# Kernel optimization log

Measured on AMD Instinct MI355X. Metric: run time of the kernel, lower is better.

## Reference

```python
import jax, jax.numpy as jnp
import numpy as np

B, F, ND, NE = 1024, 1024, 256, 256

def setup_inputs() -> dict:
    key = jax.random.key(0)
    k1, k2, k3 = jax.random.split(key, 3)
    x = jax.random.normal(k1, (B, F), dtype=jnp.float32)
    # xavier-uniform-like init scale for (F+1, units)
    lim_d = float(np.sqrt(6.0 / (F + 1 + ND)))
    lim_e = float(np.sqrt(6.0 / (F + 1 + NE)))
    dilations = jax.random.uniform(k2, (F + 1, ND), minval=-lim_d, maxval=lim_d, dtype=jnp.float32)
    erosions = jax.random.uniform(k3, (F + 1, NE), minval=-lim_e, maxval=lim_e, dtype=jnp.float32)
    return {"x": x, "dilations": dilations, "erosions": erosions}

def reference(x, dilations, erosions):
    b = x.shape[0]
    # append a zero 'bias' feature -> (b, F+1)
    xb = jnp.concatenate([x, jnp.zeros((b, 1), dtype=x.dtype)], axis=1)
    # tropical matmuls: max-plus (dilation), min-minus (erosion)
    dilated = jnp.max(xb[:, :, None] + dilations[None, :, :], axis=1)   # (b, ND)
    eroded = jnp.min(xb[:, :, None] - erosions[None, :, :], axis=1)     # (b, NE)
    return jnp.concatenate([eroded, dilated], axis=1)
```

## Files before the change

kernel.cpp:

```cpp
#include <hip/hip_runtime.h>
#include <math.h>

#define BB   1024
#define FF   1024
#define NOUT 512
#define NW   256
#define BT   128
#define NT   64
#define KT   32

__global__ __launch_bounds__(256, 2) void trop_main(
    const float* __restrict__ x,
    const float* __restrict__ dil,
    const float* __restrict__ ero,
    float* __restrict__ dst,
    int ks, int ch, int direct)
{
    const int bx = blockIdx.x;
    const int by = blockIdx.y;
    const int bz = blockIdx.z;
    const bool is_ero = (bx < (NW / NT));
    const float* __restrict__ w = is_ero ? ero : dil;
    const int c0w = is_ero ? bx * NT : bx * NT - NW;
    const int r0 = by * BT;
    const float sgn = is_ero ? -1.0f : 1.0f;

    __shared__ float lds_x[KT][BT];
    __shared__ float lds_w[KT][NT];

    const int tid = threadIdx.x;
    const int cg = tid & 7;
    const int rg = tid >> 3;

    float acc[4][8];
#pragma unroll
    for (int i = 0; i < 4; ++i)
#pragma unroll
        for (int j = 0; j < 8; ++j) acc[i][j] = -INFINITY;

    const int fstart = bz * ch;
    const int nchunk = ch / KT;

    for (int kc = 0; kc < nchunk; ++kc) {
        const int fb = fstart + kc * KT;

#pragma unroll
        for (int it = 0; it < 4; ++it) {
            const int tt = tid + it * 256;
            const int r = tt & 127;
            const int g = tt >> 7;
            const float4 v = *(const float4*)(x + (size_t)(r0 + r) * FF + fb + g * 4);
            lds_x[g * 4 + 0][r] = sgn * v.x;
            lds_x[g * 4 + 1][r] = sgn * v.y;
            lds_x[g * 4 + 2][r] = sgn * v.z;
            lds_x[g * 4 + 3][r] = sgn * v.w;
        }
#pragma unroll
        for (int it = 0; it < 2; ++it) {
            const int tt = tid + it * 256;
            const int f = tt >> 4;
            const int c4 = tt & 15;
            *(float4*)&lds_w[f][c4 * 4] =
                *(const float4*)(w + (size_t)(fb + f) * NW + c0w + c4 * 4);
        }
        __syncthreads();

#pragma unroll
        for (int ff = 0; ff < KT; ff += 2) {
            const float4 x0 = *(const float4*)&lds_x[ff][rg << 2];
            const float4 x1 = *(const float4*)&lds_x[ff + 1][rg << 2];
            const float4 wa0 = *(const float4*)&lds_w[ff][cg << 3];
            const float4 wb0 = *(const float4*)&lds_w[ff][(cg << 3) + 4];
            const float4 wa1 = *(const float4*)&lds_w[ff + 1][cg << 3];
            const float4 wb1 = *(const float4*)&lds_w[ff + 1][(cg << 3) + 4];
            const float xr0[4] = {x0.x, x0.y, x0.z, x0.w};
            const float xr1[4] = {x1.x, x1.y, x1.z, x1.w};
            const float wc0[8] = {wa0.x, wa0.y, wa0.z, wa0.w, wb0.x, wb0.y, wb0.z, wb0.w};
            const float wc1[8] = {wa1.x, wa1.y, wa1.z, wa1.w, wb1.x, wb1.y, wb1.z, wb1.w};
#pragma unroll
            for (int i = 0; i < 4; ++i)
#pragma unroll
                for (int j = 0; j < 8; ++j) {
                    acc[i][j] = fmaxf(acc[i][j],
                                      fmaxf(xr0[i] + wc0[j], xr1[i] + wc1[j]));
                }
        }
        __syncthreads();
    }

    if (bz == ks - 1) {
        const float4 ba = *(const float4*)(w + (size_t)FF * NW + c0w + (cg << 3));
        const float4 bb = *(const float4*)(w + (size_t)FF * NW + c0w + (cg << 3) + 4);
        const float bc[8] = {ba.x, ba.y, ba.z, ba.w, bb.x, bb.y, bb.z, bb.w};
#pragma unroll
        for (int i = 0; i < 4; ++i)
#pragma unroll
            for (int j = 0; j < 8; ++j) acc[i][j] = fmaxf(acc[i][j], bc[j]);
    }

    float* base = direct ? dst : dst + (size_t)bz * (BB * NOUT);
    const int cglob = bx * NT + (cg << 3);
#pragma unroll
    for (int i = 0; i < 4; ++i) {
        const int row = r0 + (rg << 2) + i;
        float4 v0, v1;
        v0.x = sgn * acc[i][0]; v0.y = sgn * acc[i][1];
        v0.z = sgn * acc[i][2]; v0.w = sgn * acc[i][3];
        v1.x = sgn * acc[i][4]; v1.y = sgn * acc[i][5];
        v1.z = sgn * acc[i][6]; v1.w = sgn * acc[i][7];
        *(float4*)(base + (size_t)row * NOUT + cglob) = v0;
        *(float4*)(base + (size_t)row * NOUT + cglob + 4) = v1;
    }
}

__global__ __launch_bounds__(256) void trop_combine(
    const float* __restrict__ ws, float* __restrict__ out, int ks)
{
    const int i4 = blockIdx.x * blockDim.x + threadIdx.x;
    const int col4 = (i4 << 2) & (NOUT - 1);
    const bool ero = col4 < NW;
    const int stride4 = BB * NOUT / 4;
    float4 v = ((const float4*)ws)[i4];
    for (int z = 1; z < ks; ++z) {
        const float4 u = ((const float4*)ws)[(size_t)z * stride4 + i4];
        if (ero) {
            v.x = fminf(v.x, u.x); v.y = fminf(v.y, u.y);
            v.z = fminf(v.z, u.z); v.w = fminf(v.w, u.w);
        } else {
            v.x = fmaxf(v.x, u.x); v.y = fmaxf(v.y, u.y);
            v.z = fmaxf(v.z, u.z); v.w = fmaxf(v.w, u.w);
        }
    }
    ((float4*)out)[i4] = v;
}

extern "C" void kernel_launch(void* const* d_in, const int* in_sizes, int n_in,
                              void* d_out, int out_size, void* d_ws, size_t ws_size,
                              hipStream_t stream) {
    const float* x = (const float*)d_in[0];
    const float* dil = (const float*)d_in[1];
    const float* ero = (const float*)d_in[2];
    float* out = (float*)d_out;

    const size_t outbytes = (size_t)BB * NOUT * sizeof(float);
    int ks = 1;
    if (ws_size >= 8 * outbytes) ks = 8;
    else if (ws_size >= 4 * outbytes) ks = 4;
    else if (ws_size >= 2 * outbytes) ks = 2;

    if (ks > 1) {
        dim3 grid(NOUT / NT, BB / BT, ks);
        trop_main<<<grid, 256, 0, stream>>>(x, dil, ero, (float*)d_ws, ks, FF / ks, 0);
        const int n4 = BB * NOUT / 4;
        trop_combine<<<n4 / 256, 256, 0, stream>>>((const float*)d_ws, out, ks);
    } else {
        dim3 grid(NOUT / NT, BB / BT, 1);
        trop_main<<<grid, 256, 0, stream>>>(x, dil, ero, out, 1, FF, 1);
    }
}
```

Measured before the change: 90.91 us.

## Replace split-K workspace and combine pass with atomic min/max into output

```diff
diff --git a/kernel.cpp b/kernel.cpp
--- a/kernel.cpp
+++ b/kernel.cpp
@@ -8,22 +8,38 @@
 #define BT   128
 #define NT   64
 #define KT   32
+#define KS   16
+#define CH   (FF / KS)
+#define NCHUNK (CH / KT)
 
-__global__ __launch_bounds__(256, 2) void trop_main(
+__device__ __forceinline__ void atomMaxF(float* p, float v) {
+    if (v >= 0.0f) atomicMax((int*)p, __float_as_int(v));
+    else           atomicMin((unsigned int*)p, __float_as_uint(v));
+}
+__device__ __forceinline__ void atomMinF(float* p, float v) {
+    if (v >= 0.0f) atomicMin((int*)p, __float_as_int(v));
+    else           atomicMax((unsigned int*)p, __float_as_uint(v));
+}
+
+__global__ __launch_bounds__(256) void trop_init(float* __restrict__ out) {
+    const int i4 = blockIdx.x * 256 + threadIdx.x;
+    const int col = (i4 << 2) & (NOUT - 1);
+    const float v = (col < NW) ? INFINITY : -INFINITY;
+    float4 o; o.x = v; o.y = v; o.z = v; o.w = v;
+    ((float4*)out)[i4] = o;
+}
+
+template <bool IS_ERO>
+__global__ __launch_bounds__(256, 4) void trop_main(
     const float* __restrict__ x,
-    const float* __restrict__ dil,
-    const float* __restrict__ ero,
-    float* __restrict__ dst,
-    int ks, int ch, int direct)
+    const float* __restrict__ w,
+    float* __restrict__ out)
 {
     const int bx = blockIdx.x;
     const int by = blockIdx.y;
     const int bz = blockIdx.z;
-    const bool is_ero = (bx < (NW / NT));
-    const float* __restrict__ w = is_ero ? ero : dil;
-    const int c0w = is_ero ? bx * NT : bx * NT - NW;
+    const int c0w = bx * NT;
     const int r0 = by * BT;
-    const float sgn = is_ero ? -1.0f : 1.0f;
 
     __shared__ float lds_x[KT][BT];
     __shared__ float lds_w[KT][NT];
@@ -38,10 +54,10 @@
 #pragma unroll
         for (int j = 0; j < 8; ++j) acc[i][j] = -INFINITY;
 
-    const int fstart = bz * ch;
-    const int nchunk = ch / KT;
+    const int fstart = bz * CH;
 
-    for (int kc = 0; kc < nchunk; ++kc) {
+#pragma unroll
+    for (int kc = 0; kc < NCHUNK; ++kc) {
         const int fb = fstart + kc * KT;
 
 #pragma unroll
@@ -50,10 +66,10 @@
             const int r = tt & 127;
             const int g = tt >> 7;
             const float4 v = *(const float4*)(x + (size_t)(r0 + r) * FF + fb + g * 4);
-            lds_x[g * 4 + 0][r] = sgn * v.x;
-            lds_x[g * 4 + 1][r] = sgn * v.y;
-            lds_x[g * 4 + 2][r] = sgn * v.z;
-            lds_x[g * 4 + 3][r] = sgn * v.w;
+            lds_x[g * 4 + 0][r] = v.x;
+            lds_x[g * 4 + 1][r] = v.y;
+            lds_x[g * 4 + 2][r] = v.z;
+            lds_x[g * 4 + 3][r] = v.w;
         }
 #pragma unroll
         for (int it = 0; it < 2; ++it) {
@@ -81,14 +97,18 @@
             for (int i = 0; i < 4; ++i)
 #pragma unroll
                 for (int j = 0; j < 8; ++j) {
-                    acc[i][j] = fmaxf(acc[i][j],
-                                      fmaxf(xr0[i] + wc0[j], xr1[i] + wc1[j]));
+                    if (IS_ERO)
+                        acc[i][j] = fmaxf(acc[i][j],
+                                          fmaxf(wc0[j] - xr0[i], wc1[j] - xr1[i]));
+                    else
+                        acc[i][j] = fmaxf(acc[i][j],
+                                          fmaxf(xr0[i] + wc0[j], xr1[i] + wc1[j]));
                 }
         }
         __syncthreads();
     }
 
-    if (bz == ks - 1) {
+    if (bz == KS - 1) {
         const float4 ba = *(const float4*)(w + (size_t)FF * NW + c0w + (cg << 3));
         const float4 bb = *(const float4*)(w + (size_t)FF * NW + c0w + (cg << 3) + 4);
         const float bc[8] = {ba.x, ba.y, ba.z, ba.w, bb.x, bb.y, bb.z, bb.w};
@@ -98,40 +118,17 @@
             for (int j = 0; j < 8; ++j) acc[i][j] = fmaxf(acc[i][j], bc[j]);
     }
 
-    float* base = direct ? dst : dst + (size_t)bz * (BB * NOUT);
-    const int cglob = bx * NT + (cg << 3);
+    const int cglob = (IS_ERO ? 0 : NW) + c0w + (cg << 3);
 #pragma unroll
     for (int i = 0; i < 4; ++i) {
         const int row = r0 + (rg << 2) + i;
-        float4 v0, v1;
-        v0.x = sgn * acc[i][0]; v0.y = sgn * acc[i][1];
-        v0.z = sgn * acc[i][2]; v0.w = sgn * acc[i][3];
-        v1.x = sgn * acc[i][4]; v1.y = sgn * acc[i][5];
-        v1.z = sgn * acc[i][6]; v1.w = sgn * acc[i][7];
-        *(float4*)(base + (size_t)row * NOUT + cglob) = v0;
-        *(float4*)(base + (size_t)row * NOUT + cglob + 4) = v1;
-    }
-}
-
-__global__ __launch_bounds__(256) void trop_combine(
-    const float* __restrict__ ws, float* __restrict__ out, int ks)
-{
-    const int i4 = blockIdx.x * blockDim.x + threadIdx.x;
-    const int col4 = (i4 << 2) & (NOUT - 1);
-    const bool ero = col4 < NW;
-    const int stride4 = BB * NOUT / 4;
-    float4 v = ((const float4*)ws)[i4];
-    for (int z = 1; z < ks; ++z) {
-        const float4 u = ((const float4*)ws)[(size_t)z * stride4 + i4];
-        if (ero) {
-            v.x = fminf(v.x, u.x); v.y = fminf(v.y, u.y);
-            v.z = fminf(v.z, u.z); v.w = fminf(v.w, u.w);
-        } else {
-            v.x = fmaxf(v.x, u.x); v.y = fmaxf(v.y, u.y);
-            v.z = fmaxf(v.z, u.z); v.w = fmaxf(v.w, u.w);
+        float* p = out + (size_t)row * NOUT + cglob;
+#pragma unroll
+        for (int j = 0; j < 8; ++j) {
+            if (IS_ERO) atomMinF(p + j, -acc[i][j]);
+            else        atomMaxF(p + j,  acc[i][j]);
         }
     }
-    ((float4*)out)[i4] = v;
 }
 
 extern "C" void kernel_launch(void* const* d_in, const int* in_sizes, int n_in,
@@ -142,19 +139,9 @@
     const float* ero = (const float*)d_in[2];
     float* out = (float*)d_out;
 
-    const size_t outbytes = (size_t)BB * NOUT * sizeof(float);
-    int ks = 1;
-    if (ws_size >= 8 * outbytes) ks = 8;
-    else if (ws_size >= 4 * outbytes) ks = 4;
-    else if (ws_size >= 2 * outbytes) ks = 2;
+    trop_init<<<BB * NOUT / 4 / 256, 256, 0, stream>>>(out);
 
-    if (ks > 1) {
-        dim3 grid(NOUT / NT, BB / BT, ks);
-        trop_main<<<grid, 256, 0, stream>>>(x, dil, ero, (float*)d_ws, ks, FF / ks, 0);
-        const int n4 = BB * NOUT / 4;
-        trop_combine<<<n4 / 256, 256, 0, stream>>>((const float*)d_ws, out, ks);
-    } else {
-        dim3 grid(NOUT / NT, BB / BT, 1);
-        trop_main<<<grid, 256, 0, stream>>>(x, dil, ero, out, 1, FF, 1);
-    }
+    dim3 grid(NW / NT, BB / BT, KS);
+    trop_main<true ><<<grid, 256, 0, stream>>>(x, ero, out);
+    trop_main<false><<<grid, 256, 0, stream>>>(x, dil, out);
 }
```

Result: slower. 244.0 us (+168.4%).

## Use 128x128 tiles with full split-K over 16 slices and swizzled LDS

Applied to the files above, without the earlier changes.

```diff
diff --git a/kernel.cpp b/kernel.cpp
--- a/kernel.cpp
+++ b/kernel.cpp
@@ -6,122 +6,122 @@
 #define NOUT 512
 #define NW   256
 #define BT   128
-#define NT   64
-#define KT   32
+#define CT   128
+#define KT   64
+#define KS   (FF / KT)
 
 __global__ __launch_bounds__(256, 2) void trop_main(
     const float* __restrict__ x,
     const float* __restrict__ dil,
     const float* __restrict__ ero,
-    float* __restrict__ dst,
-    int ks, int ch, int direct)
+    float* __restrict__ ws)
 {
     const int bx = blockIdx.x;
     const int by = blockIdx.y;
     const int bz = blockIdx.z;
-    const bool is_ero = (bx < (NW / NT));
+    const bool is_ero = (bx < 2);
     const float* __restrict__ w = is_ero ? ero : dil;
-    const int c0w = is_ero ? bx * NT : bx * NT - NW;
+    const int c0w = (bx & 1) * CT;
     const int r0 = by * BT;
     const float sgn = is_ero ? -1.0f : 1.0f;
+    const int fb = bz * KT;
 
     __shared__ float lds_x[KT][BT];
-    __shared__ float lds_w[KT][NT];
+    __shared__ float lds_w[KT][CT];
 
     const int tid = threadIdx.x;
-    const int cg = tid & 7;
-    const int rg = tid >> 3;
+    const int cg = tid & 15;
+    const int rg = tid >> 4;
 
-    float acc[4][8];
 #pragma unroll
-    for (int i = 0; i < 4; ++i)
+    for (int it = 0; it < 8; ++it) {
+        const int idx = it * 256 + tid;
+        const int r = idx >> 4;
+        const int g = idx & 15;
+        const float4 v = *(const float4*)(x + (size_t)(r0 + r) * FF + fb + g * 4);
+        const int rb = r >> 3, rl = r & 7;
+        const float vv[4] = {v.x, v.y, v.z, v.w};
+#pragma unroll
+        for (int q = 0; q < 4; ++q) {
+            const int f = g * 4 + q;
+            lds_x[f][((rb ^ (f & 15)) << 3) | rl] = sgn * vv[q];
+        }
+    }
+#pragma unroll
+    for (int it = 0; it < 8; ++it) {
+        const int idx = it * 256 + tid;
+        const int f = idx >> 5;
+        const int c4 = idx & 31;
+        *(float4*)&lds_w[f][c4 * 4] =
+            *(const float4*)(w + (size_t)(fb + f) * NW + c0w + c4 * 4);
+    }
+    __syncthreads();
+
+    float acc[8][8];
+#pragma unroll
+    for (int i = 0; i < 8; ++i)
 #pragma unroll
         for (int j = 0; j < 8; ++j) acc[i][j] = -INFINITY;
 
-    const int fstart = bz * ch;
-    const int nchunk = ch / KT;
-
-    for (int kc = 0; kc < nchunk; ++kc) {
-        const int fb = fstart + kc * KT;
-
+#pragma unroll 2
+    for (int ff = 0; ff < KT; ff += 2) {
+        const int s0 = ((rg ^ (ff & 15)) << 3);
+        const int s1 = ((rg ^ ((ff + 1) & 15)) << 3);
+        const float4 xa0 = *(const float4*)&lds_x[ff][s0];
+        const float4 xb0 = *(const float4*)&lds_x[ff][s0 + 4];
+        const float4 xa1 = *(const float4*)&lds_x[ff + 1][s1];
+        const float4 xb1 = *(const float4*)&lds_x[ff + 1][s1 + 4];
+        const float4 wa0 = *(const float4*)&lds_w[ff][cg * 4];
+        const float4 wb0 = *(const float4*)&lds_w[ff][64 + cg * 4];
+        const float4 wa1 = *(const float4*)&lds_w[ff + 1][cg * 4];
+        const float4 wb1 = *(const float4*)&lds_w[ff + 1][64 + cg * 4];
+        const float xr0[8] = {xa0.x, xa0.y, xa0.z, xa0.w, xb0.x, xb0.y, xb0.z, xb0.w};
+        const float xr1[8] = {xa1.x, xa1.y, xa1.z, xa1.w, xb1.x, xb1.y, xb1.z, xb1.w};
+        const float wc0[8] = {wa0.x, wa0.y, wa0.z, wa0.w, wb0.x, wb0.y, wb0.z, wb0.w};
+        const float wc1[8] = {wa1.x, wa1.y, wa1.z, wa1.w, wb1.x, wb1.y, wb1.z, wb1.w};
 #pragma unroll
-        for (int it = 0; it < 4; ++it) {
-            const int tt = tid + it * 256;
-            const int r = tt & 127;
-            const int g = tt >> 7;
-            const float4 v = *(const float4*)(x + (size_t)(r0 + r) * FF + fb + g * 4);
-            lds_x[g * 4 + 0][r] = sgn * v.x;
-            lds_x[g * 4 + 1][r] = sgn * v.y;
-            lds_x[g * 4 + 2][r] = sgn * v.z;
-            lds_x[g * 4 + 3][r] = sgn * v.w;
-        }
+        for (int i = 0; i < 8; ++i)
 #pragma unroll
-        for (int it = 0; it < 2; ++it) {
-            const int tt = tid + it * 256;
-            const int f = tt >> 4;
-            const int c4 = tt & 15;
-            *(float4*)&lds_w[f][c4 * 4] =
-                *(const float4*)(w + (size_t)(fb + f) * NW + c0w + c4 * 4);
-        }
-        __syncthreads();
-
-#pragma unroll
-        for (int ff = 0; ff < KT; ff += 2) {
-            const float4 x0 = *(const float4*)&lds_x[ff][rg << 2];
-            const float4 x1 = *(const float4*)&lds_x[ff + 1][rg << 2];
-            const float4 wa0 = *(const float4*)&lds_w[ff][cg << 3];
-            const float4 wb0 = *(const float4*)&lds_w[ff][(cg << 3) + 4];
-            const float4 wa1 = *(const float4*)&lds_w[ff + 1][cg << 3];
-            const float4 wb1 = *(const float4*)&lds_w[ff + 1][(cg << 3) + 4];
-            const float xr0[4] = {x0.x, x0.y, x0.z, x0.w};
-            const float xr1[4] = {x1.x, x1.y, x1.z, x1.w};
-            const float wc0[8] = {wa0.x, wa0.y, wa0.z, wa0.w, wb0.x, wb0.y, wb0.z, wb0.w};
-            const float wc1[8] = {wa1.x, wa1.y, wa1.z, wa1.w, wb1.x, wb1.y, wb1.z, wb1.w};
-#pragma unroll
-            for (int i = 0; i < 4; ++i)
-#pragma unroll
-                for (int j = 0; j < 8; ++j) {
-                    acc[i][j] = fmaxf(acc[i][j],
-                                      fmaxf(xr0[i] + wc0[j], xr1[i] + wc1[j]));
-                }
-        }
-        __syncthreads();
+            for (int j = 0; j < 8; ++j) {
+                acc[i][j] = fmaxf(acc[i][j],
+                                  fmaxf(xr0[i] + wc0[j], xr1[i] + wc1[j]));
+            }
     }
 
-    if (bz == ks - 1) {
-        const float4 ba = *(const float4*)(w + (size_t)FF * NW + c0w + (cg << 3));
-        const float4 bb = *(const float4*)(w + (size_t)FF * NW + c0w + (cg << 3) + 4);
+    if (bz == KS - 1) {
+        const float4 ba = *(const float4*)(w + (size_t)FF * NW + c0w + cg * 4);
+        const float4 bb = *(const float4*)(w + (size_t)FF * NW + c0w + 64 + cg * 4);
         const float bc[8] = {ba.x, ba.y, ba.z, ba.w, bb.x, bb.y, bb.z, bb.w};
 #pragma unroll
-        for (int i = 0; i < 4; ++i)
+        for (int i = 0; i < 8; ++i)
 #pragma unroll
             for (int j = 0; j < 8; ++j) acc[i][j] = fmaxf(acc[i][j], bc[j]);
     }
 
-    float* base = direct ? dst : dst + (size_t)bz * (BB * NOUT);
-    const int cglob = bx * NT + (cg << 3);
+    float* plane = ws + (size_t)bz * (BB * NOUT);
+    const int cglob = bx * CT + cg * 4;
 #pragma unroll
-    for (int i = 0; i < 4; ++i) {
-        const int row = r0 + (rg << 2) + i;
+    for (int i = 0; i < 8; ++i) {
+        const int row = r0 + rg * 8 + i;
         float4 v0, v1;
         v0.x = sgn * acc[i][0]; v0.y = sgn * acc[i][1];
         v0.z = sgn * acc[i][2]; v0.w = sgn * acc[i][3];
         v1.x = sgn * acc[i][4]; v1.y = sgn * acc[i][5];
         v1.z = sgn * acc[i][6]; v1.w = sgn * acc[i][7];
-        *(float4*)(base + (size_t)row * NOUT + cglob) = v0;
-        *(float4*)(base + (size_t)row * NOUT + cglob + 4) = v1;
+        *(float4*)(plane + (size_t)row * NOUT + cglob) = v0;
+        *(float4*)(plane + (size_t)row * NOUT + cglob + 64) = v1;
     }
 }
 
 __global__ __launch_bounds__(256) void trop_combine(
-    const float* __restrict__ ws, float* __restrict__ out, int ks)
+    const float* __restrict__ ws, float* __restrict__ out)
 {
-    const int i4 = blockIdx.x * blockDim.x + threadIdx.x;
-    const int col4 = (i4 << 2) & (NOUT - 1);
-    const bool ero = col4 < NW;
+    const int i4 = blockIdx.x * 256 + threadIdx.x;
+    const bool ero = (i4 & 127) < 64;
     const int stride4 = BB * NOUT / 4;
     float4 v = ((const float4*)ws)[i4];
-    for (int z = 1; z < ks; ++z) {
+#pragma unroll
+    for (int z = 1; z < KS; ++z) {
         const float4 u = ((const float4*)ws)[(size_t)z * stride4 + i4];
         if (ero) {
             v.x = fminf(v.x, u.x); v.y = fminf(v.y, u.y);
@@ -141,20 +141,9 @@
     const float* dil = (const float*)d_in[1];
     const float* ero = (const float*)d_in[2];
     float* out = (float*)d_out;
+    float* ws = (float*)d_ws;
 
-    const size_t outbytes = (size_t)BB * NOUT * sizeof(float);
-    int ks = 1;
-    if (ws_size >= 8 * outbytes) ks = 8;
-    else if (ws_size >= 4 * outbytes) ks = 4;
-    else if (ws_size >= 2 * outbytes) ks = 2;
-
-    if (ks > 1) {
-        dim3 grid(NOUT / NT, BB / BT, ks);
-        trop_main<<<grid, 256, 0, stream>>>(x, dil, ero, (float*)d_ws, ks, FF / ks, 0);
-        const int n4 = BB * NOUT / 4;
-        trop_combine<<<n4 / 256, 256, 0, stream>>>((const float*)d_ws, out, ks);
-    } else {
-        dim3 grid(NOUT / NT, BB / BT, 1);
-        trop_main<<<grid, 256, 0, stream>>>(x, dil, ero, out, 1, FF, 1);
-    }
+    dim3 grid(4, BB / BT, KS);
+    trop_main<<<grid, 256, 0, stream>>>(x, dil, ero, ws);
+    trop_combine<<<BB * NOUT / 4 / 256, 256, 0, stream>>>(ws, out);
 }
```

Result: no change. 92.35 us (+1.6%).
